# Kernel tuning notes

Measured on AMD Instinct MI355X. Metric: run time of the kernel, lower is better.

The kernel has to match this reference:

```python
import jax, jax.numpy as jnp
import numpy as np

HIDDEN = 512

def _gru_cell(x, h, W_ih, W_hh, b_ih, b_hh):
    # torch GRUCell math; gates ordered r, z, n
    gi = x @ W_ih.T + b_ih            # [B, 3H]
    gh = h @ W_hh.T + b_hh            # [B, 3H]
    i_r, i_z, i_n = jnp.split(gi, 3, axis=-1)
    h_r, h_z, h_n = jnp.split(gh, 3, axis=-1)
    r = jax.nn.sigmoid(i_r + h_r)
    z = jax.nn.sigmoid(i_z + h_z)
    n = jnp.tanh(i_n + r * h_n)
    return (1.0 - z) * n + z * h


def setup_inputs() -> dict:
    key = jax.random.key(0)
    ks = jax.random.split(key, 12)
    B, T, E, Fh, H, V = 128, 32, 300, 128, HIDDEN, 32000
    s = 0.05
    return {
        "g_feat": jax.random.normal(ks[0], (B, Fh), jnp.float32),
        "t_feat": jax.random.normal(ks[1], (B, Fh), jnp.float32),
        "lang_feat": jax.random.normal(ks[2], (B, T, E), jnp.float32),
        "lang_len": jnp.full((B,), T, dtype=jnp.int64) if jax.config.jax_enable_x64 else jnp.full((B,), T, dtype=jnp.int32),
        "W_feat": jax.random.normal(ks[3], (2 * Fh, H), jnp.float32) * s,
        "b_feat": jax.random.normal(ks[4], (H,), jnp.float32) * s,
        "W_ih": jax.random.normal(ks[5], (3 * H, E), jnp.float32) * s,
        "W_hh": jax.random.normal(ks[6], (3 * H, H), jnp.float32) * s,
        "b_ih": jax.random.normal(ks[7], (3 * H,), jnp.float32) * s,
        "b_hh": jax.random.normal(ks[8], (3 * H,), jnp.float32) * s,
        "W_cls": jax.random.normal(ks[9], (H, V), jnp.float32) * s,
        "b_cls": jax.random.normal(ks[10], (V,), jnp.float32) * s,
    }


def reference(g_feat, t_feat, lang_feat, lang_len, W_feat, b_feat,
              W_ih, W_hh, b_ih, b_hh, W_cls, b_cls):
    # forward_train_batch (is_eval=False), feat_input add_target=True
    inp_feat = jnp.concatenate((g_feat, t_feat), axis=1)      # [B, feat_size]
    hidden0 = jax.nn.relu(inp_feat @ W_feat + b_feat)          # [B, H]
    num_words = lang_feat.shape[1]                             # == lang_len[0], static
    xs = jnp.swapaxes(lang_feat[:, : num_words - 1, :], 0, 1)  # [T-1, B, E] teacher forcing

    def step(h, x):
        h = _gru_cell(x, h, W_ih, W_hh, b_ih, b_hh)
        logits = h @ W_cls + b_cls                             # [B, V]
        return h, logits

    _, logits = jax.lax.scan(step, hidden0, xs)                # [T-1, B, V]
    return jnp.swapaxes(logits, 0, 1)                          # lang_cap: [B, T-1, V]
```

## Files before the change

kernel.cpp:

```cpp
#include <hip/hip_runtime.h>
#include <hip/hip_bf16.h>
#include <cstdint>
#include <cstddef>

typedef __attribute__((ext_vector_type(8))) short short8;
typedef __attribute__((ext_vector_type(4))) float f32x4;


__global__ __launch_bounds__(512) void k_hidden0(
    const float* __restrict__ g_feat, const float* __restrict__ t_feat,
    const float* __restrict__ W_feat, const float* __restrict__ b_feat,
    float* __restrict__ h_cur) {
  __shared__ float inp[256];
  const int b = blockIdx.x;
  const int tid = threadIdx.x;
  if (tid < 128) inp[tid] = g_feat[b * 128 + tid];
  else if (tid < 256) inp[tid] = t_feat[b * 128 + tid - 128];
  __syncthreads();
  float acc = b_feat[tid];
#pragma unroll 8
  for (int k = 0; k < 256; ++k) acc = fmaf(inp[k], W_feat[k * 512 + tid], acc);
  h_cur[b * 512 + tid] = fmaxf(acc, 0.f);
}

__global__ __launch_bounds__(256) void k_gi(
    const float* __restrict__ lang, const float* __restrict__ W_ih,
    const float* __restrict__ b_ih, const float* __restrict__ b_hh,
    float* __restrict__ gi_all) {
  __shared__ float As[16][65];
  __shared__ float Bs[16][65];
  const int n0 = blockIdx.x * 64;
  const int m0 = blockIdx.y * 64;
  const int tid = threadIdx.x;
  const int tx = tid & 15, ty = tid >> 4;
  float acc[4][4] = {};
  for (int k0 = 0; k0 < 300; k0 += 16) {
    const int kk = tid & 15;
    const int r0 = tid >> 4;
    const int kg = k0 + kk;
    const bool kv = kg < 300;
#pragma unroll
    for (int i = 0; i < 4; ++i) {
      int row = r0 + i * 16;
      int r = m0 + row;
      int t = r >> 7, b = r & 127;
      As[kk][row] = kv ? lang[(size_t)b * 9600 + t * 300 + kg] : 0.f;
    }
#pragma unroll
    for (int i = 0; i < 4; ++i) {
      int n = r0 + i * 16;
      Bs[kk][n] = kv ? W_ih[(size_t)(n0 + n) * 300 + kg] : 0.f;
    }
    __syncthreads();
#pragma unroll
    for (int k = 0; k < 16; ++k) {
      float a[4], b[4];
#pragma unroll
      for (int i = 0; i < 4; ++i) a[i] = As[k][ty * 4 + i];
#pragma unroll
      for (int j = 0; j < 4; ++j) b[j] = Bs[k][tx * 4 + j];
#pragma unroll
      for (int i = 0; i < 4; ++i)
#pragma unroll
        for (int j = 0; j < 4; ++j) acc[i][j] = fmaf(a[i], b[j], acc[i][j]);
    }
    __syncthreads();
  }
#pragma unroll
  for (int i = 0; i < 4; ++i) {
    int r = m0 + ty * 4 + i;
#pragma unroll
    for (int j = 0; j < 4; ++j) {
      int c = n0 + tx * 4 + j;
      gi_all[(size_t)r * 1536 + c] =
          acc[i][j] + b_ih[c] + (c < 1024 ? b_hh[c] : 0.f);
    }
  }
}

__global__ __launch_bounds__(256) void k_gh(
    const float* __restrict__ h_cur, const float* __restrict__ W_hh,
    float* __restrict__ gh_part) {
  __shared__ float As[16][65];
  __shared__ float Bs[16][36];
  const int n0 = blockIdx.x * 32;
  const int m0 = blockIdx.y * 64;
  const int kz = blockIdx.z;
  const int tid = threadIdx.x;
  const int tx = tid & 7, ty = tid >> 3;
  float acc[2][4] = {};
  for (int kt = 0; kt < 8; ++kt) {
    const int kbase = kz * 128 + kt * 16;
    const int kk = tid & 15, r0 = tid >> 4;
#pragma unroll
    for (int i = 0; i < 4; ++i) {
      int row = r0 + i * 16;
      As[kk][row] = h_cur[(size_t)(m0 + row) * 512 + kbase + kk];
    }
#pragma unroll
    for (int i = 0; i < 2; ++i) {
      int n = r0 + i * 16;
      Bs[kk][n] = W_hh[(size_t)(n0 + n) * 512 + kbase + kk];
    }
    __syncthreads();
#pragma unroll
    for (int k = 0; k < 16; ++k) {
      float a0 = As[k][ty * 2], a1 = As[k][ty * 2 + 1];
      float b[4];
#pragma unroll
      for (int j = 0; j < 4; ++j) b[j] = Bs[k][tx * 4 + j];
#pragma unroll
      for (int j = 0; j < 4; ++j) {
        acc[0][j] = fmaf(a0, b[j], acc[0][j]);
        acc[1][j] = fmaf(a1, b[j], acc[1][j]);
      }
    }
    __syncthreads();
  }
  float* dst = gh_part + (size_t)kz * (128 * 1536);
#pragma unroll
  for (int i = 0; i < 2; ++i) {
    int m = m0 + ty * 2 + i;
#pragma unroll
    for (int j = 0; j < 4; ++j)
      dst[(size_t)m * 1536 + n0 + tx * 4 + j] = acc[i][j];
  }
}

__global__ __launch_bounds__(512) void k_gates(
    const float* __restrict__ gi_all, const float* __restrict__ gh_part,
    const float* __restrict__ b_hh, float* __restrict__ h_cur,
    __hip_bfloat16* __restrict__ h_all, int t) {
  const int b = blockIdx.x;
  const int j = threadIdx.x;
  const float* gi = gi_all + (size_t)(t * 128 + b) * 1536;
  float ghr = 0.f, ghz = 0.f, ghn = 0.f;
#pragma unroll
  for (int s = 0; s < 4; ++s) {
    const float* p = gh_part + (size_t)s * (128 * 1536) + (size_t)b * 1536;
    ghr += p[j];
    ghz += p[j + 512];
    ghn += p[j + 1024];
  }
  ghn += b_hh[1024 + j];
  float r = 1.f / (1.f + __expf(-(gi[j] + ghr)));
  float z = 1.f / (1.f + __expf(-(gi[j + 512] + ghz)));
  float n = tanhf(gi[j + 1024] + r * ghn);
  float h_old = h_cur[b * 512 + j];
  float hn = (1.f - z) * n + z * h_old;
  h_cur[b * 512 + j] = hn;
  h_all[((size_t)t * 128 + b) * 512 + j] = __float2bfloat16(hn);
}

__global__ __launch_bounds__(256) void k_tcls(const float* __restrict__ W,
                                              __hip_bfloat16* __restrict__ WT) {
  __shared__ float tile[32][33];
  const int v0 = blockIdx.x * 32, k0 = blockIdx.y * 32;
  const int tx = threadIdx.x & 31, ty = threadIdx.x >> 5;
#pragma unroll
  for (int i = 0; i < 32; i += 8)
    tile[ty + i][tx] = W[(size_t)(k0 + ty + i) * 32000 + v0 + tx];
  __syncthreads();
#pragma unroll
  for (int i = 0; i < 32; i += 8)
    WT[(size_t)(v0 + ty + i) * 512 + k0 + tx] = __float2bfloat16(tile[tx][ty + i]);
}

__global__ __launch_bounds__(256, 2) void k_cls_gemm(
    const __hip_bfloat16* __restrict__ Abf,
    const __hip_bfloat16* __restrict__ BTbf,
    const float* __restrict__ b_cls, float* __restrict__ out) {
  __shared__ unsigned short Al[128][72];
  __shared__ unsigned short Bl[128][72];
  const int nblk = blockIdx.x;
  const int tblk = blockIdx.y;
  const int tid = threadIdx.x;
  const int wave = tid >> 6, lane = tid & 63;
  const int quad = lane >> 4, l16 = lane & 15;
  const int mw = (wave >> 1) * 64, nw = (wave & 1) * 64;

  f32x4 acc[4][4] = {};

  const unsigned short* Ag =
      (const unsigned short*)Abf + (size_t)tblk * 128 * 512;
  const unsigned short* Bg =
      (const unsigned short*)BTbf + (size_t)nblk * 128 * 512;

  for (int k0 = 0; k0 < 512; k0 += 64) {
    __syncthreads();
#pragma unroll
    for (int i = 0; i < 4; ++i) {
      int c = tid + i * 256;
      int row = c >> 3, c8 = c & 7;
      *(uint4*)(&Al[row][c8 * 8]) =
          *(const uint4*)(Ag + (size_t)row * 512 + k0 + c8 * 8);
      *(uint4*)(&Bl[row][c8 * 8]) =
          *(const uint4*)(Bg + (size_t)row * 512 + k0 + c8 * 8);
    }
    __syncthreads();
#pragma unroll
    for (int kc = 0; kc < 2; ++kc) {
      short8 a[4], b[4];
#pragma unroll
      for (int mt = 0; mt < 4; ++mt)
        a[mt] = *(const short8*)(&Al[mw + mt * 16 + l16][kc * 32 + quad * 8]);
#pragma unroll
      for (int nt = 0; nt < 4; ++nt)
        b[nt] = *(const short8*)(&Bl[nw + nt * 16 + l16][kc * 32 + quad * 8]);
#pragma unroll
      for (int mt = 0; mt < 4; ++mt)
#pragma unroll
        for (int nt = 0; nt < 4; ++nt)
          acc[mt][nt] = __builtin_amdgcn_mfma_f32_16x16x32_bf16(
              a[mt], b[nt], acc[mt][nt], 0, 0, 0);
    }
  }
#pragma unroll
  for (int nt = 0; nt < 4; ++nt) {
    int v = nblk * 128 + nw + nt * 16 + l16;
    float bc = b_cls[v];
#pragma unroll
    for (int mt = 0; mt < 4; ++mt) {
#pragma unroll
      for (int i = 0; i < 4; ++i) {
        int m = mw + mt * 16 + quad * 4 + i;
        out[((size_t)m * 31 + tblk) * 32000 + v] = acc[mt][nt][i] + bc;
      }
    }
  }
}

extern "C" void kernel_launch(void* const* d_in, const int* in_sizes, int n_in,
                              void* d_out, int out_size, void* d_ws,
                              size_t ws_size, hipStream_t stream) {
  (void)in_sizes; (void)n_in; (void)out_size; (void)ws_size;
  const float* g_feat = (const float*)d_in[0];
  const float* t_feat = (const float*)d_in[1];
  const float* lang   = (const float*)d_in[2];
  const float* W_feat = (const float*)d_in[4];
  const float* b_feat = (const float*)d_in[5];
  const float* W_ih   = (const float*)d_in[6];
  const float* W_hh   = (const float*)d_in[7];
  const float* b_ih   = (const float*)d_in[8];
  const float* b_hh   = (const float*)d_in[9];
  const float* W_cls  = (const float*)d_in[10];
  const float* b_cls  = (const float*)d_in[11];
  float* out = (float*)d_out;

  char* ws = (char*)d_ws;
  float* h_cur   = (float*)(ws);
  float* gh_part = (float*)(ws + 262144);
  float* gi_all  = (float*)(ws + 3407872);
  __hip_bfloat16* h_all = (__hip_bfloat16*)(ws + 27787264);
  __hip_bfloat16* WT    = (__hip_bfloat16*)(ws + 31850496);

  k_hidden0<<<128, 512, 0, stream>>>(g_feat, t_feat, W_feat, b_feat, h_cur);
  k_gi<<<dim3(24, 62), 256, 0, stream>>>(lang, W_ih, b_ih, b_hh, gi_all);
  k_tcls<<<dim3(1000, 16), 256, 0, stream>>>(W_cls, WT);
  for (int t = 0; t < 31; ++t) {
    k_gh<<<dim3(48, 2, 4), 256, 0, stream>>>(h_cur, W_hh, gh_part);
    k_gates<<<128, 512, 0, stream>>>(gi_all, gh_part, b_hh, h_cur, h_all, t);
  }
  k_cls_gemm<<<dim3(250, 31), 256, 0, stream>>>(h_all, WT, b_cls, out);
}
```

Before: 1.208 ms.

## Replace per-timestep GRU launches with persistent cooperative kernel using MFMA split-bf16

Replaces the 62 per-step kernel launches of the recurrent loop with a single cooperative persistent kernel. Each block keeps its slice of W_hh in registers as hi/lo bf16 pairs and computes h@W_hh with bf16 MFMA, using hi/lo splits of both h and W to approximate fp32 precision. Blocks synchronise across timesteps with an atomic grid barrier. This removes launch overhead and repeated weight reloads, but adds a spin barrier with a timeout break and falls back to the old path if cooperative launch is unavailable.

```diff
diff --git a/kernel.cpp b/kernel.cpp
--- a/kernel.cpp
+++ b/kernel.cpp
@@ -78,6 +78,148 @@
   }
 }
 
+__global__ __launch_bounds__(256) void k_wsplit(
+    const float* __restrict__ W_hh, __hip_bfloat16* __restrict__ WBhi,
+    __hip_bfloat16* __restrict__ WBlo, unsigned int* bar) {
+  if (blockIdx.x == 0 && threadIdx.x == 0) bar[0] = 0u;
+  const int cblk = blockIdx.x & 31;
+  const int s = blockIdx.x >> 5;
+  const size_t tbase = (size_t)(cblk * 3 + s) * (16 * 64 * 8);
+  for (int e = threadIdx.x; e < 8192; e += 256) {
+    const int ks = e >> 9;
+    const int rem = e & 511;
+    const int l = rem >> 3;
+    const int j = rem & 7;
+    const int row = s * 512 + cblk * 16 + (l & 15);
+    const int k = ks * 32 + ((l >> 4) * 8) + j;
+    const float w = W_hh[(size_t)row * 512 + k];
+    const __hip_bfloat16 hi = __float2bfloat16(w);
+    const __hip_bfloat16 lo = __float2bfloat16(w - __bfloat162float(hi));
+    const size_t idx = tbase + ((size_t)ks * 64 + l) * 8 + j;
+    WBhi[idx] = hi;
+    WBlo[idx] = lo;
+  }
+}
+
+__device__ __forceinline__ void grid_barrier(unsigned int* bar,
+                                             unsigned int target) {
+  __threadfence();
+  __syncthreads();
+  if (threadIdx.x == 0) {
+    __hip_atomic_fetch_add(bar, 1u, __ATOMIC_ACQ_REL, __HIP_MEMORY_SCOPE_AGENT);
+    unsigned int spin = 0;
+    while (__hip_atomic_load(bar, __ATOMIC_RELAXED, __HIP_MEMORY_SCOPE_AGENT) <
+           target) {
+      __builtin_amdgcn_s_sleep(2);
+      if (++spin > (1u << 23)) break;
+    }
+  }
+  __syncthreads();
+  __threadfence();
+}
+
+__global__ __launch_bounds__(256, 1) void k_rnn(
+    const float* __restrict__ h0, const float* __restrict__ gi_all,
+    const __hip_bfloat16* __restrict__ WBhi,
+    const __hip_bfloat16* __restrict__ WBlo, const float* __restrict__ b_hh,
+    __hip_bfloat16* hbuf0, __hip_bfloat16* hbuf1,
+    __hip_bfloat16* __restrict__ h_all, unsigned int* bar) {
+  __shared__ float red[4][3][16][16];
+  const int tid = threadIdx.x;
+  const int bid = blockIdx.x;
+  const int cblk = bid & 31;
+  const int mt = bid >> 5;
+  const int wave = tid >> 6, lane = tid & 63;
+  const int l16 = lane & 15, quad = lane >> 4;
+  const int brow = tid >> 4, jcol = tid & 15;
+  const int bglob = mt * 16 + brow;
+  const int jglob = cblk * 16 + jcol;
+
+  short8 Bf[3][12];
+#pragma unroll
+  for (int s = 0; s < 3; ++s) {
+#pragma unroll
+    for (int ks = 0; ks < 12; ++ks) {
+      const int kg = wave * 12 + ks;
+      const unsigned short* src;
+      int ks16;
+      if (kg < 16) {
+        src = (const unsigned short*)WBhi; ks16 = kg;
+      } else if (kg < 32) {
+        src = (const unsigned short*)WBhi; ks16 = kg - 16;
+      } else {
+        src = (const unsigned short*)WBlo; ks16 = kg - 32;
+      }
+      Bf[s][ks] = *(const short8*)(
+          src + ((((size_t)(cblk * 3 + s) * 16 + ks16) * 64 + lane) * 8));
+    }
+  }
+
+  const float bhn = b_hh[1024 + jglob];
+  float h = h0[bglob * 512 + jglob];
+
+  __hip_bfloat16* cur = hbuf0;
+  __hip_bfloat16* nxt = hbuf1;
+  {
+    const __hip_bfloat16 hi = __float2bfloat16(h);
+    cur[bglob * 1024 + jglob] = hi;
+    cur[bglob * 1024 + 512 + jglob] =
+        __float2bfloat16(h - __bfloat162float(hi));
+  }
+  unsigned int target = 256;
+  grid_barrier(bar, target);
+
+  for (int t = 0; t < 31; ++t) {
+    const float* gi = gi_all + ((size_t)(t * 128 + bglob)) * 1536 + jglob;
+    const float gir = gi[0];
+    const float giz = gi[512];
+    const float gin = gi[1024];
+
+    f32x4 acc0 = {0.f, 0.f, 0.f, 0.f};
+    f32x4 acc1 = {0.f, 0.f, 0.f, 0.f};
+    f32x4 acc2 = {0.f, 0.f, 0.f, 0.f};
+    const unsigned short* arow =
+        (const unsigned short*)cur + (size_t)(mt * 16 + l16) * 1024;
+    const int cbase = wave * 384 + quad * 8;
+#pragma unroll
+    for (int ks = 0; ks < 12; ++ks) {
+      const int c = (cbase + ks * 32) & 1023;
+      const short8 a = *(const short8*)(arow + c);
+      acc0 = __builtin_amdgcn_mfma_f32_16x16x32_bf16(a, Bf[0][ks], acc0, 0, 0, 0);
+      acc1 = __builtin_amdgcn_mfma_f32_16x16x32_bf16(a, Bf[1][ks], acc1, 0, 0, 0);
+      acc2 = __builtin_amdgcn_mfma_f32_16x16x32_bf16(a, Bf[2][ks], acc2, 0, 0, 0);
+    }
+    *(f32x4*)&red[wave][0][l16][quad * 4] = acc0;
+    *(f32x4*)&red[wave][1][l16][quad * 4] = acc1;
+    *(f32x4*)&red[wave][2][l16][quad * 4] = acc2;
+    __syncthreads();
+    float ghr = 0.f, ghz = 0.f, ghn = 0.f;
+#pragma unroll
+    for (int w = 0; w < 4; ++w) {
+      ghr += red[w][0][jcol][brow];
+      ghz += red[w][1][jcol][brow];
+      ghn += red[w][2][jcol][brow];
+    }
+    ghn += bhn;
+    const float r = 1.f / (1.f + __expf(-(gir + ghr)));
+    const float z = 1.f / (1.f + __expf(-(giz + ghz)));
+    const float n = tanhf(gin + r * ghn);
+    h = (1.f - z) * n + z * h;
+
+    const __hip_bfloat16 hi = __float2bfloat16(h);
+    nxt[bglob * 1024 + jglob] = hi;
+    nxt[bglob * 1024 + 512 + jglob] =
+        __float2bfloat16(h - __bfloat162float(hi));
+    h_all[((size_t)(t * 128 + bglob)) * 512 + jglob] = hi;
+
+    if (t < 30) {
+      target += 256;
+      grid_barrier(bar, target);
+      __hip_bfloat16* tmp = cur; cur = nxt; nxt = tmp;
+    }
+  }
+}
+
 __global__ __launch_bounds__(256) void k_gh(
     const float* __restrict__ h_cur, const float* __restrict__ W_hh,
     float* __restrict__ gh_part) {
@@ -248,18 +390,48 @@
   float* out = (float*)d_out;
 
   char* ws = (char*)d_ws;
-  float* h_cur   = (float*)(ws);
-  float* gh_part = (float*)(ws + 262144);
-  float* gi_all  = (float*)(ws + 3407872);
-  __hip_bfloat16* h_all = (__hip_bfloat16*)(ws + 27787264);
-  __hip_bfloat16* WT    = (__hip_bfloat16*)(ws + 31850496);
+  float* h_cur          = (float*)(ws);
+  unsigned int* bar     = (unsigned int*)(ws + 262144);
+  __hip_bfloat16* WBhi  = (__hip_bfloat16*)(ws + 262400);
+  __hip_bfloat16* WBlo  = (__hip_bfloat16*)(ws + 1835264);
+  float* gh_part        = (float*)(ws + 262400);
+  __hip_bfloat16* hbuf0 = (__hip_bfloat16*)(ws + 3408128);
+  __hip_bfloat16* hbuf1 = (__hip_bfloat16*)(ws + 3670272);
+  float* gi_all         = (float*)(ws + 3932416);
+  __hip_bfloat16* h_all = (__hip_bfloat16*)(ws + 28311808);
+  __hip_bfloat16* WT    = (__hip_bfloat16*)(ws + 32375040);
 
   k_hidden0<<<128, 512, 0, stream>>>(g_feat, t_feat, W_feat, b_feat, h_cur);
   k_gi<<<dim3(24, 62), 256, 0, stream>>>(lang, W_ih, b_ih, b_hh, gi_all);
   k_tcls<<<dim3(1000, 16), 256, 0, stream>>>(W_cls, WT);
-  for (int t = 0; t < 31; ++t) {
-    k_gh<<<dim3(48, 2, 4), 256, 0, stream>>>(h_cur, W_hh, gh_part);
-    k_gates<<<128, 512, 0, stream>>>(gi_all, gh_part, b_hh, h_cur, h_all, t);
+
+  static int coop_ok = -1;
+  if (coop_ok < 0) {
+    int v = 0;
+    int dev = 0;
+    hipGetDevice(&dev);
+    if (hipDeviceGetAttribute(&v, hipDeviceAttributeCooperativeLaunch, dev) !=
+        hipSuccess)
+      v = 0;
+    coop_ok = v;
+  }
+  bool did_coop = false;
+  if (coop_ok == 1) {
+    k_wsplit<<<96, 256, 0, stream>>>(W_hh, WBhi, WBlo, bar);
+    const float* h0c = h_cur;
+    void* kargs[] = {(void*)&h0c,   (void*)&gi_all, (void*)&WBhi,
+                     (void*)&WBlo,  (void*)&b_hh,   (void*)&hbuf0,
+                     (void*)&hbuf1, (void*)&h_all,  (void*)&bar};
+    hipError_t e = hipLaunchCooperativeKernel(
+        reinterpret_cast<void*>(k_rnn), dim3(256), dim3(256), kargs, 0,
+        stream);
+    did_coop = (e == hipSuccess);
+  }
+  if (!did_coop) {
+    for (int t = 0; t < 31; ++t) {
+      k_gh<<<dim3(48, 2, 4), 256, 0, stream>>>(h_cur, W_hh, gh_part);
+      k_gates<<<128, 512, 0, stream>>>(gi_all, gh_part, b_hh, h_cur, h_all, t);
+    }
   }
   k_cls_gemm<<<dim3(250, 31), 256, 0, stream>>>(h_all, WT, b_cls, out);
 }
```

New measurement: 2.426 ms. +100.8%, slower.
